# Performance work log

Hardware: AMD Instinct MI355X
Metric: run time of the kernel (lower is better)

Reference implementation:

```python
import jax, jax.numpy as jnp
import numpy as np

N_NODES = 50000
N_EDGES = 1_600_000
D_FEAT = 128


def setup_inputs() -> dict:
    key = jax.random.key(0)
    k1, k2, k3 = jax.random.split(key, 3)
    x = jax.random.normal(k1, (N_NODES, D_FEAT), dtype=jnp.float32)
    # Valid CSR rowptr: sorted, rowptr[0] = 0, rowptr[-1] = N_EDGES.
    inner = jnp.sort(jax.random.randint(k2, (N_NODES - 1,), 0, N_EDGES + 1))
    rowptr = jnp.concatenate([
        jnp.zeros((1,), jnp.int64) if False else jnp.array([0], dtype=jnp.int32),
        inner.astype(jnp.int32),
        jnp.array([N_EDGES], dtype=jnp.int32),
    ]).astype(jnp.int64)
    col = jax.random.randint(k3, (N_EDGES,), 0, N_NODES).astype(jnp.int64)
    return {"x": x, "rowptr": rowptr, "col": col}


def reference(x, rowptr, col):
    """CSR SpMM with sum aggregation: out[i] = sum_{j in [rowptr[i], rowptr[i+1])} x[col[j]]."""
    n_nodes = rowptr.shape[0] - 1
    n_edges = col.shape[0]
    # Recover row id of each edge from rowptr (jit-friendly, no dynamic repeat).
    row = jnp.searchsorted(rowptr, jnp.arange(n_edges, dtype=rowptr.dtype), side="right") - 1
    gathered = x[col]  # [E, D]
    out = jax.ops.segment_sum(gathered, row, num_segments=n_nodes)  # [N, D]
    return out
```

## Files before the change

### kernel.cpp

```cpp
#include <hip/hip_runtime.h>


typedef float f32x4 __attribute__((ext_vector_type(4)));
typedef unsigned int u32;

__global__ __launch_bounds__(256) void cvt_bf16_kernel(
    const float2* __restrict__ x2, u32* __restrict__ xb, int npairs)
{
    for (int i = blockIdx.x * 256 + threadIdx.x; i < npairs; i += gridDim.x * 256) {
        const float2 f = x2[i];
        u32 a = __float_as_uint(f.x);
        a = (a + 0x7FFFu + ((a >> 16) & 1u)) >> 16;
        u32 b = __float_as_uint(f.y);
        b = (b + 0x7FFFu + ((b >> 16) & 1u)) & 0xFFFF0000u;
        xb[i] = a | b;
    }
}

__device__ __forceinline__ void addv(float* acc, const uint4 v) {
    acc[0] += __uint_as_float(v.x << 16);
    acc[1] += __uint_as_float(v.x & 0xFFFF0000u);
    acc[2] += __uint_as_float(v.y << 16);
    acc[3] += __uint_as_float(v.y & 0xFFFF0000u);
    acc[4] += __uint_as_float(v.z << 16);
    acc[5] += __uint_as_float(v.z & 0xFFFF0000u);
    acc[6] += __uint_as_float(v.w << 16);
    acc[7] += __uint_as_float(v.w & 0xFFFF0000u);
}

__global__ __launch_bounds__(256) void spmm_rowwave_kernel(
    const uint4* __restrict__ xb,
    const int*   __restrict__ rowptr,
    const int*   __restrict__ col,
    float*       __restrict__ out,
    int n_nodes)
{
    const int wave = threadIdx.x >> 6;
    const int lane = threadIdx.x & 63;
    const int sub  = lane >> 4;
    const int l16  = lane & 15;
    const int row  = blockIdx.x * 4 + wave;
    if (row >= n_nodes) return;

    const uint4* xbl = xb + l16;
    const int r0 = rowptr[row];
    const int r1 = rowptr[row + 1];

    float acc[8] = {0.f, 0.f, 0.f, 0.f, 0.f, 0.f, 0.f, 0.f};

    int j = r0;
    for (; j + 16 <= r1; j += 16) {
        const int c0 = __builtin_nontemporal_load(col + j + sub + 0);
        const int c1 = __builtin_nontemporal_load(col + j + sub + 4);
        const int c2 = __builtin_nontemporal_load(col + j + sub + 8);
        const int c3 = __builtin_nontemporal_load(col + j + sub + 12);
        const uint4 v0 = xbl[(size_t)c0 * 16];
        const uint4 v1 = xbl[(size_t)c1 * 16];
        const uint4 v2 = xbl[(size_t)c2 * 16];
        const uint4 v3 = xbl[(size_t)c3 * 16];
        addv(acc, v0); addv(acc, v1); addv(acc, v2); addv(acc, v3);
    }
    for (; j + 4 <= r1; j += 4) {
        const int c = __builtin_nontemporal_load(col + j + sub);
        addv(acc, xbl[(size_t)c * 16]);
    }
    if (j + sub < r1) {
        const int c = __builtin_nontemporal_load(col + j + sub);
        addv(acc, xbl[(size_t)c * 16]);
    }

    #pragma unroll
    for (int k = 0; k < 8; ++k) {
        acc[k] += __shfl_xor(acc[k], 16, 64);
        acc[k] += __shfl_xor(acc[k], 32, 64);
    }

    if (sub == 0) {
        float* dst = out + (size_t)row * 128 + l16 * 8;
        __builtin_nontemporal_store((f32x4){acc[0], acc[1], acc[2], acc[3]}, (f32x4*)dst);
        __builtin_nontemporal_store((f32x4){acc[4], acc[5], acc[6], acc[7]}, (f32x4*)(dst + 4));
    }
}

__global__ __launch_bounds__(256) void spmm_f32_kernel(
    const f32x4* __restrict__ x4,
    const int*   __restrict__ rowptr,
    const int*   __restrict__ col,
    f32x4*       __restrict__ out4,
    int n_nodes)
{
    const int lane = threadIdx.x & 31;
    const int grp  = threadIdx.x >> 5;
    const int row  = blockIdx.x * 8 + grp;
    if (row >= n_nodes) return;

    const int r1 = rowptr[row + 1];
    int j = rowptr[row];
    f32x4 acc = {0.f, 0.f, 0.f, 0.f};
    for (; j + 4 <= r1; j += 4) {
        const int c0 = col[j + 0];
        const int c1 = col[j + 1];
        const int c2 = col[j + 2];
        const int c3 = col[j + 3];
        f32x4 a = x4[(size_t)c0 * 32 + lane];
        f32x4 b = x4[(size_t)c1 * 32 + lane];
        f32x4 c = x4[(size_t)c2 * 32 + lane];
        f32x4 d = x4[(size_t)c3 * 32 + lane];
        acc += a; acc += b; acc += c; acc += d;
    }
    for (; j < r1; ++j) acc += x4[(size_t)col[j] * 32 + lane];
    out4[(size_t)row * 32 + lane] = acc;
}

extern "C" void kernel_launch(void* const* d_in, const int* in_sizes, int n_in,
                              void* d_out, int out_size, void* d_ws, size_t ws_size,
                              hipStream_t stream) {
    const float* x      = (const float*)d_in[0];
    const int*   rowptr = (const int*)d_in[1];
    const int*   col    = (const int*)d_in[2];
    float*       out    = (float*)d_out;

    const int n_nodes = in_sizes[1] - 1;
    const int n_feats = (n_nodes > 0) ? in_sizes[0] / n_nodes : 0;
    const size_t xb_bytes = (size_t)in_sizes[0] * 2;

    if (ws_size >= xb_bytes && n_feats == 128) {
        u32* xb = (u32*)d_ws;
        const int npairs = in_sizes[0] / 2;
        cvt_bf16_kernel<<<2048, 256, 0, stream>>>((const float2*)x, xb, npairs);
        const int blocks = (n_nodes + 3) / 4;
        spmm_rowwave_kernel<<<blocks, 256, 0, stream>>>(
            (const uint4*)xb, rowptr, col, out, n_nodes);
    } else {
        const int blocks = (n_nodes + 7) / 8;
        spmm_f32_kernel<<<blocks, 256, 0, stream>>>(
            (const f32x4*)x, rowptr, col, (f32x4*)out, n_nodes);
    }
}
```

Baseline: 66.77 us.

## Split bf16 features into four column chunks assigned to blocks by XCD

The conversion kernel now writes bf16 features in a chunk-major layout, four 32-feature chunks each stored contiguously across all nodes. The SpMM kernel launches four times as many blocks, and blockIdx&3 picks the chunk. With round-robin block dispatch across XCDs, each XCD should then gather from a working set a quarter the size, improving L2 hit rates. In exchange, every row's col indices and rowptr are read four times, and each gather is only 8 bytes per lane, so there are more, smaller memory transactions.

```diff
diff --git a/kernel.cpp b/kernel.cpp
--- a/kernel.cpp
+++ b/kernel.cpp
@@ -4,81 +4,80 @@
 typedef float f32x4 __attribute__((ext_vector_type(4)));
 typedef unsigned int u32;
 
-__global__ __launch_bounds__(256) void cvt_bf16_kernel(
-    const float2* __restrict__ x2, u32* __restrict__ xb, int npairs)
+#define NCHUNK 4
+
+__global__ __launch_bounds__(256) void cvt_t_kernel(
+    const float2* __restrict__ x2, u32* __restrict__ xt, int n_nodes)
 {
-    for (int i = blockIdx.x * 256 + threadIdx.x; i < npairs; i += gridDim.x * 256) {
-        const float2 f = x2[i];
+    const int total = n_nodes * 64;
+    for (int p = blockIdx.x * 256 + threadIdx.x; p < total; p += gridDim.x * 256) {
+        const float2 f = x2[p];
         u32 a = __float_as_uint(f.x);
         a = (a + 0x7FFFu + ((a >> 16) & 1u)) >> 16;
         u32 b = __float_as_uint(f.y);
         b = (b + 0x7FFFu + ((b >> 16) & 1u)) & 0xFFFF0000u;
-        xb[i] = a | b;
+        const int node = p >> 6, pr = p & 63;
+        const int c = pr >> 4, k = pr & 15;
+        xt[((size_t)c * n_nodes + node) * 16 + k] = a | b;
     }
 }
 
-__device__ __forceinline__ void addv(float* acc, const uint4 v) {
+__device__ __forceinline__ void addv2(float* acc, const uint2 v) {
     acc[0] += __uint_as_float(v.x << 16);
     acc[1] += __uint_as_float(v.x & 0xFFFF0000u);
     acc[2] += __uint_as_float(v.y << 16);
     acc[3] += __uint_as_float(v.y & 0xFFFF0000u);
-    acc[4] += __uint_as_float(v.z << 16);
-    acc[5] += __uint_as_float(v.z & 0xFFFF0000u);
-    acc[6] += __uint_as_float(v.w << 16);
-    acc[7] += __uint_as_float(v.w & 0xFFFF0000u);
 }
 
-__global__ __launch_bounds__(256) void spmm_rowwave_kernel(
-    const uint4* __restrict__ xb,
+__global__ __launch_bounds__(256) void spmm_xcd_kernel(
+    const uint2* __restrict__ xt,
     const int*   __restrict__ rowptr,
     const int*   __restrict__ col,
     float*       __restrict__ out,
     int n_nodes)
 {
-    const int wave = threadIdx.x >> 6;
-    const int lane = threadIdx.x & 63;
-    const int sub  = lane >> 4;
-    const int l16  = lane & 15;
-    const int row  = blockIdx.x * 4 + wave;
+    const int wave   = threadIdx.x >> 6;
+    const int lane   = threadIdx.x & 63;
+    const int sub    = lane >> 3;
+    const int l8     = lane & 7;
+    const int chunk  = blockIdx.x & 3;
+    const int rowgrp = blockIdx.x >> 2;
+    const int row    = rowgrp * 4 + wave;
     if (row >= n_nodes) return;
 
-    const uint4* xbl = xb + l16;
-    const int r0 = rowptr[row];
+    const uint2* xc = xt + (size_t)chunk * n_nodes * 8 + l8;
+
     const int r1 = rowptr[row + 1];
+    int j = rowptr[row];
+    float acc[4] = {0.f, 0.f, 0.f, 0.f};
 
-    float acc[8] = {0.f, 0.f, 0.f, 0.f, 0.f, 0.f, 0.f, 0.f};
-
-    int j = r0;
     for (; j + 16 <= r1; j += 16) {
-        const int c0 = __builtin_nontemporal_load(col + j + sub + 0);
-        const int c1 = __builtin_nontemporal_load(col + j + sub + 4);
-        const int c2 = __builtin_nontemporal_load(col + j + sub + 8);
-        const int c3 = __builtin_nontemporal_load(col + j + sub + 12);
-        const uint4 v0 = xbl[(size_t)c0 * 16];
-        const uint4 v1 = xbl[(size_t)c1 * 16];
-        const uint4 v2 = xbl[(size_t)c2 * 16];
-        const uint4 v3 = xbl[(size_t)c3 * 16];
-        addv(acc, v0); addv(acc, v1); addv(acc, v2); addv(acc, v3);
+        const int c0 = __builtin_nontemporal_load(col + j + sub);
+        const int c1 = __builtin_nontemporal_load(col + j + 8 + sub);
+        const uint2 v0 = xc[(size_t)c0 * 8];
+        const uint2 v1 = xc[(size_t)c1 * 8];
+        addv2(acc, v0); addv2(acc, v1);
     }
-    for (; j + 4 <= r1; j += 4) {
+    for (; j + 8 <= r1; j += 8) {
         const int c = __builtin_nontemporal_load(col + j + sub);
-        addv(acc, xbl[(size_t)c * 16]);
+        addv2(acc, xc[(size_t)c * 8]);
     }
     if (j + sub < r1) {
         const int c = __builtin_nontemporal_load(col + j + sub);
-        addv(acc, xbl[(size_t)c * 16]);
+        addv2(acc, xc[(size_t)c * 8]);
     }
 
     #pragma unroll
-    for (int k = 0; k < 8; ++k) {
+    for (int k = 0; k < 4; ++k) {
+        acc[k] += __shfl_xor(acc[k], 8, 64);
         acc[k] += __shfl_xor(acc[k], 16, 64);
         acc[k] += __shfl_xor(acc[k], 32, 64);
     }
 
     if (sub == 0) {
-        float* dst = out + (size_t)row * 128 + l16 * 8;
-        __builtin_nontemporal_store((f32x4){acc[0], acc[1], acc[2], acc[3]}, (f32x4*)dst);
-        __builtin_nontemporal_store((f32x4){acc[4], acc[5], acc[6], acc[7]}, (f32x4*)(dst + 4));
+        float* dst = out + (size_t)row * 128 + chunk * 32 + l8 * 4;
+        __builtin_nontemporal_store((f32x4){acc[0], acc[1], acc[2], acc[3]},
+                                    (f32x4*)dst);
     }
 }
 
@@ -125,12 +124,12 @@
     const size_t xb_bytes = (size_t)in_sizes[0] * 2;
 
     if (ws_size >= xb_bytes && n_feats == 128) {
-        u32* xb = (u32*)d_ws;
-        const int npairs = in_sizes[0] / 2;
-        cvt_bf16_kernel<<<2048, 256, 0, stream>>>((const float2*)x, xb, npairs);
-        const int blocks = (n_nodes + 3) / 4;
-        spmm_rowwave_kernel<<<blocks, 256, 0, stream>>>(
-            (const uint4*)xb, rowptr, col, out, n_nodes);
+        u32* xt = (u32*)d_ws;
+        cvt_t_kernel<<<2048, 256, 0, stream>>>((const float2*)x, xt, n_nodes);
+        const int rowgrps = (n_nodes + 3) / 4;
+        const int blocks  = rowgrps * NCHUNK;
+        spmm_xcd_kernel<<<blocks, 256, 0, stream>>>(
+            (const uint2*)xt, rowptr, col, out, n_nodes);
     } else {
         const int blocks = (n_nodes + 7) / 8;
         spmm_f32_kernel<<<blocks, 256, 0, stream>>>(
```

New measurement: 118.1 us. 1.77x slower.
